# Kernel tuning notes

Hardware: AMD Instinct MI355X
Metric: run time of the kernel (lower is better)

## Reference

```python
import jax, jax.numpy as jnp
import numpy as np
import math

D_MODEL = 1024
NUM_HEADS = 16
D_HEAD = D_MODEL // NUM_HEADS          # 64
N_FREQ = D_HEAD // 2 + 1               # 33 rfft bins
COMPRESSION_RATIO = 0.5


def setup_inputs() -> dict:
    key = jax.random.key(0)
    k_x, k_qkv, k_out, k_b, k_m = jax.random.split(key, 5)
    B, S = 2, 2048
    x = jax.random.normal(k_x, (B, S, D_MODEL), dtype=jnp.float32)
    # Linear weights stored as [in, out] (torch Linear uses [out, in]; math identical).
    w_qkv = jax.random.normal(k_qkv, (D_MODEL, 3 * D_MODEL), dtype=jnp.float32) / math.sqrt(D_MODEL)
    w_out = jax.random.normal(k_out, (D_MODEL, D_MODEL), dtype=jnp.float32) / math.sqrt(D_MODEL)
    b_out = jax.random.normal(k_b, (D_MODEL,), dtype=jnp.float32) * 0.01
    # Learned per-frequency-bin mask logits of AdaptiveFrequencyMask(d_state=d_head).
    # Initialized around logit(compression_ratio) with small noise.
    init_logit = math.log(COMPRESSION_RATIO / (1.0 - COMPRESSION_RATIO))
    mask_logits = init_logit + 0.1 * jax.random.normal(k_m, (N_FREQ,), dtype=jnp.float32)
    return {"x": x, "w_qkv": w_qkv, "w_out": w_out, "b_out": b_out, "mask_logits": mask_logits}


def _spectral_filter(t, mask):
    # rfft over d_head dim, apply learned soft mask, inverse rfft.  t: [B,H,S,dh]
    tf = jnp.fft.rfft(t, axis=-1)          # [B,H,S,N_FREQ] complex
    tf = tf * mask                          # broadcast real mask over bins
    return jnp.fft.irfft(tf, n=t.shape[-1], axis=-1).astype(t.dtype)


def reference(x, w_qkv, w_out, b_out, mask_logits):
    B, S, D = x.shape
    H, dh = NUM_HEADS, D_HEAD
    qkv = x @ w_qkv                                         # [B,S,3D]
    q, k, v = jnp.split(qkv, 3, axis=-1)
    # [B,S,D] -> [B,H,S,dh]
    to_heads = lambda t: t.reshape(B, S, H, dh).transpose(0, 2, 1, 3)
    q, k, v = to_heads(q), to_heads(k), to_heads(v)
    mask = jax.nn.sigmoid(mask_logits)                      # [N_FREQ]
    q = _spectral_filter(q, mask)
    k = _spectral_filter(k, mask)
    scores = jnp.einsum('bhqd,bhkd->bhqk', q, k) / math.sqrt(dh)
    attn = jax.nn.softmax(scores, axis=-1)                  # dropout p=0 (eval)
    out = jnp.einsum('bhqk,bhkd->bhqd', attn, v)
    out = out.transpose(0, 2, 1, 3).reshape(B, S, D)
    return out @ w_out + b_out
```

## Files before the change

kernel.cpp:

```cpp
#include <hip/hip_runtime.h>

#define S_LEN 2048
#define NH    16
#define DH    64
#define DM    1024
#define NQKV  3072

typedef __attribute__((ext_vector_type(8))) __bf16 bf16x8;
typedef __attribute__((ext_vector_type(4))) float  f32x4;
typedef unsigned short ushort_t;

static __device__ __forceinline__ unsigned short bf16b(float f) {
  return __builtin_bit_cast(unsigned short, (__bf16)f);
}

static __device__ __forceinline__ float exp2v(float x) {
  return __builtin_amdgcn_exp2f(x);
}

static __device__ __forceinline__ bf16x8 pack8(float4 f0, float4 f1) {
  uint4 v;
  v.x = ((unsigned)bf16b(f0.y) << 16) | bf16b(f0.x);
  v.y = ((unsigned)bf16b(f0.w) << 16) | bf16b(f0.z);
  v.z = ((unsigned)bf16b(f1.y) << 16) | bf16b(f1.x);
  v.w = ((unsigned)bf16b(f1.w) << 16) | bf16b(f1.z);
  return __builtin_bit_cast(bf16x8, v);
}

static __device__ __forceinline__ void glds16(const void* g, void* l) {
  __builtin_amdgcn_global_load_lds((const __attribute__((address_space(1))) unsigned int*)g,
                                   (__attribute__((address_space(3))) unsigned int*)l, 16, 0, 0);
}

#define OFF_WT  65536ull
#define OFF_WOT 6356992ull
#define OFF_Q   8454144ull
#define OFF_K   16842752ull
#define OFF_V   25231360ull
#define OFF_AO  33619968ull

__global__ __launch_bounds__(256) void k_prep(const float* __restrict__ wqkv,
                                              const float* __restrict__ wout,
                                              const float* __restrict__ x,
                                              const float* __restrict__ logits,
                                              unsigned short* __restrict__ Wt,
                                              unsigned short* __restrict__ Wot,
                                              unsigned short* __restrict__ xb) {
  __shared__ __align__(16) char sbuf[16640];
  int bid = blockIdx.x;
  int t = threadIdx.x;

  if (bid < 256) {
    float* msk = (float*)sbuf;
    float* Kd  = (float*)(sbuf + 144);
    ushort_t (*Fb)[72] = (ushort_t(*)[72])(sbuf + 416);
    if (t < 33) msk[t] = 1.0f / (1.0f + __expf(-logits[t]));
    __syncthreads();
    if (t < 64) {
      float acc = msk[0];
      #pragma unroll
      for (int f = 1; f < 32; ++f) {
        int r = (f * t) & 63;
        acc += 2.0f * msk[f] * __cosf((float)r * (6.28318530717958647692f / 64.0f));
      }
      acc += msk[32] * ((t & 1) ? -1.0f : 1.0f);
      Kd[t] = acc * (1.0f / 64.0f);
    }
    __syncthreads();
    for (int idx = t; idx < 4096; idx += 256) {
      int j = idx >> 6, i = idx & 63;
      Fb[j][i] = bf16b(Kd[(j - i) & 63]);
    }
    __syncthreads();

    int lane = t & 63, w = t >> 6;
    int m16 = lane & 15, quad = lane >> 4;
    int kx = bid >> 5, yy = bid & 31;
    int which = yy >> 4, h = yy & 15;
    int base = which * 1024 + h * 64;

    bf16x8 af0 = *(const bf16x8*)(&Fb[w * 16 + m16][quad * 8]);
    bf16x8 af1 = *(const bf16x8*)(&Fb[w * 16 + m16][32 + quad * 8]);

    f32x4 acc[8] = {};
    #pragma unroll 2
    for (int n = 0; n < 8; ++n) {
      const float* Wg = wqkv + (size_t)(kx * 128 + n * 16 + m16) * NQKV + base + quad * 8;
      float4 a0 = *(const float4*)(Wg);
      float4 a1 = *(const float4*)(Wg + 4);
      float4 b0 = *(const float4*)(Wg + 32);
      float4 b1 = *(const float4*)(Wg + 36);
      acc[n] = __builtin_amdgcn_mfma_f32_16x16x32_bf16(af0, pack8(a0, a1), acc[n], 0, 0, 0);
      acc[n] = __builtin_amdgcn_mfma_f32_16x16x32_bf16(af1, pack8(b0, b1), acc[n], 0, 0, 0);
    }
    float sc = (which == 0) ? 0.18033688011112042f : 1.0f;
    #pragma unroll
    for (int n = 0; n < 8; ++n) {
      #pragma unroll
      for (int r = 0; r < 4; ++r) {
        int j = w * 16 + quad * 4 + r;
        Wt[(size_t)(base + j) * DM + kx * 128 + n * 16 + m16] = bf16b(acc[n][r] * sc);
      }
    }
  } else if (bid < 768) {
    float (*Ts)[65] = (float(*)[65])sbuf;
    int b1 = bid - 256;
    if (b1 < 256) {
      int kt = b1 & 15, nt = b1 >> 4;
      int cb = 2048 + nt * 64, kbase = kt * 64;
      #pragma unroll
      for (int p = 0; p < 16; ++p) {
        int kk = p * 4 + (t >> 6);
        Ts[kk][t & 63] = wqkv[(size_t)(kbase + kk) * NQKV + cb + (t & 63)];
      }
      __syncthreads();
      #pragma unroll
      for (int p = 0; p < 16; ++p) {
        int nn = p * 4 + (t >> 6);
        Wt[(size_t)(cb + nn) * DM + kbase + (t & 63)] = bf16b(Ts[t & 63][nn]);
      }
    } else {
      int b2 = b1 - 256;
      int kt = b2 & 15, nt = b2 >> 4;
      int cb = nt * 64, kbase = kt * 64;
      #pragma unroll
      for (int p = 0; p < 16; ++p) {
        int kk = p * 4 + (t >> 6);
        Ts[kk][t & 63] = wout[(size_t)(kbase + kk) * DM + cb + (t & 63)];
      }
      __syncthreads();
      #pragma unroll
      for (int p = 0; p < 16; ++p) {
        int nn = p * 4 + (t >> 6);
        Wot[(size_t)(cb + nn) * DM + kbase + (t & 63)] = bf16b(Ts[t & 63][nn]);
      }
    }
  } else {
    size_t i = ((size_t)(bid - 768) * 256 + t) * 8;
    const float4* xp = (const float4*)(x + i);
    float4 a = xp[0], b = xp[1];
    uint4 v;
    v.x = ((unsigned)bf16b(a.y) << 16) | bf16b(a.x);
    v.y = ((unsigned)bf16b(a.w) << 16) | bf16b(a.z);
    v.z = ((unsigned)bf16b(b.y) << 16) | bf16b(b.x);
    v.w = ((unsigned)bf16b(b.w) << 16) | bf16b(b.z);
    *(uint4*)(xb + i) = v;
  }
}

template<int BM, int BN, int WCOLS, int MR, int NR>
__device__ __forceinline__ void gemm_core2(const unsigned short* __restrict__ A,
                                           const unsigned short* __restrict__ Bw,
                                           int bm, int bn, unsigned short* smem,
                                           f32x4 (&acc)[MR][NR]) {
  constexpr int SLOT = (BM + BN) * 64;
  constexpr int PA = BM / 64, PB = BN / 64;
  constexpr int L = PA + PB;
  int t = threadIdx.x, lane = t & 63, w = t >> 6;
  int m16 = lane & 15, quad = lane >> 4;
  int wr = (w / WCOLS) * (MR * 16), wc = (w % WCOLS) * (NR * 16);
  int xr = m16 & 7;
  int trow = t >> 3, tcol = t & 7;
  int gsw = (tcol ^ (trow & 7)) * 8;
  const unsigned short* Ag = A  + (size_t)(bm * BM + trow) * DM + gsw;
  const unsigned short* Bg = Bw + (size_t)(bn * BN + trow) * DM + gsw;
  unsigned short* Al = smem + trow * 64 + tcol * 8;
  unsigned short* Bl = smem + BM * 64 + trow * 64 + tcol * 8;

  #pragma unroll
  for (int s = 0; s < 2; ++s) {
    #pragma unroll
    for (int p = 0; p < PA; ++p)
      glds16(Ag + (size_t)p * 64 * DM + s * 64, Al + s * SLOT + p * 4096);
    #pragma unroll
    for (int p = 0; p < PB; ++p)
      glds16(Bg + (size_t)p * 64 * DM + s * 64, Bl + s * SLOT + p * 4096);
  }

  #pragma unroll 1
  for (int ks = 0; ks < 16; ++ks) {
    if (ks < 15) asm volatile("s_waitcnt vmcnt(%0)" :: "n"(L) : "memory");
    else         asm volatile("s_waitcnt vmcnt(0)" ::: "memory");
    __builtin_amdgcn_s_barrier();
    __builtin_amdgcn_sched_barrier(0);
    const unsigned short* As = smem + (ks & 1) * SLOT;
    const unsigned short* Bs = As + BM * 64;
    #pragma unroll
    for (int kk = 0; kk < 2; ++kk) {
      bf16x8 af[MR], bfr[NR];
      #pragma unroll
      for (int i = 0; i < MR; ++i)
        af[i] = *(const bf16x8*)(As + (wr + i * 16 + m16) * 64 + ((kk * 4 + quad) ^ xr) * 8);
      #pragma unroll
      for (int j = 0; j < NR; ++j)
        bfr[j] = *(const bf16x8*)(Bs + (wc + j * 16 + m16) * 64 + ((kk * 4 + quad) ^ xr) * 8);
      #pragma unroll
      for (int i = 0; i < MR; ++i)
        #pragma unroll
        for (int j = 0; j < NR; ++j)
          acc[i][j] = __builtin_amdgcn_mfma_f32_16x16x32_bf16(af[i], bfr[j], acc[i][j], 0, 0, 0);
    }
    if (ks < 14) {
      __builtin_amdgcn_s_barrier();
      __builtin_amdgcn_sched_barrier(0);
      int kn = ks + 2;
      #pragma unroll
      for (int p = 0; p < PA; ++p)
        glds16(Ag + (size_t)p * 64 * DM + kn * 64, Al + (ks & 1) * SLOT + p * 4096);
      #pragma unroll
      for (int p = 0; p < PB; ++p)
        glds16(Bg + (size_t)p * 64 * DM + kn * 64, Bl + (ks & 1) * SLOT + p * 4096);
    }
  }
  __syncthreads();
}

__global__ __launch_bounds__(512, 1) void k_gemm_qkv(const unsigned short* __restrict__ xb,
                                                     const unsigned short* __restrict__ Bw,
                                                     unsigned short* __restrict__ Qb,
                                                     unsigned short* __restrict__ Kb,
                                                     unsigned short* __restrict__ Vt) {
  __shared__ __align__(16) unsigned short smem[65536];
  f32x4 acc[8][4] = {};
  int bn = blockIdx.x, bm = blockIdx.y;
  gemm_core2<256, 256, 4, 8, 4>(xb, Bw, bm, bn, smem, acc);

  int t = threadIdx.x, lane = t & 63, w = t >> 6;
  int m16 = lane & 15, quad = lane >> 4;
  int b = bm >> 3, srow = (bm & 7) * 256;
  int which = bn >> 2;
  ushort_t (*Tr)[264] = (ushort_t(*)[264])smem;

  if (which < 2) {
    unsigned short* dstB = which ? Kb : Qb;
    int hbase = (bn & 3) * 4;
    #pragma unroll
    for (int ch = 0; ch < 2; ++ch) {
      if ((w >> 2) == ch) {
        #pragma unroll
        for (int i = 0; i < 8; ++i)
          #pragma unroll
          for (int j = 0; j < 4; ++j)
            #pragma unroll
            for (int r = 0; r < 4; ++r)
              Tr[i * 16 + quad * 4 + r][(w & 3) * 64 + j * 16 + m16] = bf16b(acc[i][j][r]);
      }
      __syncthreads();
      int row = t >> 2, qh = t & 3;
      unsigned short* dst = dstB +
          ((size_t)(b * 16 + hbase + qh) * 2048 + srow + ch * 128 + row) * 64;
      #pragma unroll
      for (int p = 0; p < 8; ++p)
        *(uint4*)(dst + p * 8) = *(const uint4*)(&Tr[row][qh * 64 + p * 8]);
      __syncthreads();
    }
  } else {
    int hb = (bn - 8) * 4;
    #pragma unroll
    for (int ch = 0; ch < 2; ++ch) {
      if (((w >> 1) & 1) == ch) {
        #pragma unroll
        for (int i = 0; i < 8; ++i)
          #pragma unroll
          for (int j = 0; j < 4; ++j)
            #pragma unroll
            for (int r = 0; r < 4; ++r)
              Tr[(w & 1) * 64 + j * 16 + m16][(w >> 2) * 128 + i * 16 + quad * 4 + r] =
                  bf16b(acc[i][j][r]);
      }
      __syncthreads();
      int c = t >> 2, qh = t & 3;
      int h = hb + ch * 2 + (c >> 6), d = c & 63;
      unsigned short* dst = Vt + ((size_t)(b * 16 + h) * 64 + d) * 2048 + srow;
      #pragma unroll
      for (int p = 0; p < 8; ++p)
        *(uint4*)(dst + qh * 64 + p * 8) = *(const uint4*)(&Tr[c][qh * 64 + p * 8]);
      __syncthreads();
    }
  }
}

__global__ __launch_bounds__(512, 2) void k_attn(const unsigned short* __restrict__ Qb,
                                                 const unsigned short* __restrict__ Kb,
                                                 const unsigned short* __restrict__ Vt,
                                                 unsigned short* __restrict__ AO) {
  __shared__ __align__(16) unsigned short smem[65536];
  int t = threadIdx.x;
  int w = t >> 6, lane = t & 63;
  int m16 = lane & 15, quad = lane >> 4;
  int bid = blockIdx.x;
  int jj = bid >> 3;
  int bh = ((jj & 3) << 3) + (bid & 7);
  int qbase = (jj >> 2) * 256 + w * 32;

  const unsigned short* QpA = Qb + ((size_t)bh * S_LEN + qbase + m16) * DH + quad * 8;
  const unsigned short* QpB = QpA + 16 * DH;
  bf16x8 aq0A = *(const bf16x8*)(QpA);
  bf16x8 aq1A = *(const bf16x8*)(QpA + 32);
  bf16x8 aq0B = *(const bf16x8*)(QpB);
  bf16x8 aq1B = *(const bf16x8*)(QpB + 32);
  const unsigned short* Kbase = Kb + (size_t)bh * S_LEN * DH;
  const unsigned short* Vbase = Vt + (size_t)bh * DH * S_LEN;

  int xr = m16 & 7;
  unsigned short* Pw = smem + 32768 + w * 4096;

  int trow = t >> 3;
  int tcol = t & 7;
  int gswz = tcol ^ (trow & 7);
  const unsigned short* Kg = Kbase + (size_t)trow * 64 + gswz * 8;
  const unsigned short* Vg = Vbase + (size_t)trow * S_LEN + gswz * 8;
  unsigned short* Kl = smem + trow * 64 + tcol * 8;
  unsigned short* Vl = smem + 16384 + trow * 64 + tcol * 8;

  f32x4 oA[4] = {}, oB[4] = {};
  float lA = 0.f, lB = 0.f;
  f32x4 zero = {0.f, 0.f, 0.f, 0.f};

  #pragma unroll
  for (int tt = 0; tt < 4; ++tt) {
    glds16(Kg + (size_t)tt * 4096, Kl + tt * 4096);
    glds16(Vg + tt * 64,           Vl + tt * 4096);
  }

  #pragma unroll 1
  for (int wnd = 0; wnd < 16; ++wnd) {
    if (wnd < 15) asm volatile("s_waitcnt vmcnt(4)" ::: "memory");
    else          asm volatile("s_waitcnt vmcnt(0)" ::: "memory");
    __builtin_amdgcn_s_barrier();
    __builtin_amdgcn_sched_barrier(0);
    int sb = (wnd & 1) << 1;
    const unsigned short* Ka  = smem + sb * 4096;
    const unsigned short* Kbs = smem + (sb + 1) * 4096;
    const unsigned short* Va  = smem + 16384 + sb * 4096;
    const unsigned short* Vbs = smem + 16384 + (sb + 1) * 4096;
    unsigned short* Pa = Pw;
    unsigned short* Pb = Pw + 2048;

    f32x4 saA[4], saB[4];
    #pragma unroll
    for (int g = 0; g < 4; ++g) {
      int rk = g * 16 + m16;
      bf16x8 kf0 = *(const bf16x8*)(Ka + rk * 64 + ((quad ^ xr) * 8));
      bf16x8 kf1 = *(const bf16x8*)(Ka + rk * 64 + (((4 + quad) ^ xr) * 8));
      saA[g] = __builtin_amdgcn_mfma_f32_16x16x32_bf16(kf0, aq0A, zero, 0, 0, 0);
      saA[g] = __builtin_amdgcn_mfma_f32_16x16x32_bf16(kf1, aq1A, saA[g], 0, 0, 0);
      saB[g] = __builtin_amdgcn_mfma_f32_16x16x32_bf16(kf0, aq0B, zero, 0, 0, 0);
      saB[g] = __builtin_amdgcn_mfma_f32_16x16x32_bf16(kf1, aq1B, saB[g], 0, 0, 0);
    }
    #pragma unroll
    for (int g = 0; g < 4; ++g) {
      int chw = (((2 * g + (quad >> 1)) ^ xr) << 3) + ((quad & 1) << 2);
      float a0 = exp2v(saA[g][0]), a1 = exp2v(saA[g][1]);
      float a2 = exp2v(saA[g][2]), a3 = exp2v(saA[g][3]);
      lA += (a0 + a1) + (a2 + a3);
      uint2 pka;
      pka.x = ((unsigned)bf16b(a1) << 16) | bf16b(a0);
      pka.y = ((unsigned)bf16b(a3) << 16) | bf16b(a2);
      *(uint2*)(Pa + m16 * 64 + chw) = pka;
      float b0 = exp2v(saB[g][0]), b1 = exp2v(saB[g][1]);
      float b2 = exp2v(saB[g][2]), b3 = exp2v(saB[g][3]);
      lB += (b0 + b1) + (b2 + b3);
      uint2 pkb;
      pkb.x = ((unsigned)bf16b(b1) << 16) | bf16b(b0);
      pkb.y = ((unsigned)bf16b(b3) << 16) | bf16b(b2);
      *(uint2*)(Pa + (16 + m16) * 64 + chw) = pkb;
    }
    f32x4 sbA[4], sbB[4];
    #pragma unroll
    for (int g = 0; g < 4; ++g) {
      int rk = g * 16 + m16;
      bf16x8 kf0 = *(const bf16x8*)(Kbs + rk * 64 + ((quad ^ xr) * 8));
      bf16x8 kf1 = *(const bf16x8*)(Kbs + rk * 64 + (((4 + quad) ^ xr) * 8));
      sbA[g] = __builtin_amdgcn_mfma_f32_16x16x32_bf16(kf0, aq0A, zero, 0, 0, 0);
      sbA[g] = __builtin_amdgcn_mfma_f32_16x16x32_bf16(kf1, aq1A, sbA[g], 0, 0, 0);
      sbB[g] = __builtin_amdgcn_mfma_f32_16x16x32_bf16(kf0, aq0B, zero, 0, 0, 0);
      sbB[g] = __builtin_amdgcn_mfma_f32_16x16x32_bf16(kf1, aq1B, sbB[g], 0, 0, 0);
    }
    #pragma unroll
    for (int c = 0; c < 2; ++c) {
      bf16x8 apA = *(const bf16x8*)(Pa + m16 * 64 + (((4 * c + quad) ^ xr) << 3));
      bf16x8 apB = *(const bf16x8*)(Pa + (16 + m16) * 64 + (((4 * c + quad) ^ xr) << 3));
      #pragma unroll
      for (int j = 0; j < 4; ++j) {
        int dv = j * 16 + m16;
        bf16x8 bv = *(const bf16x8*)(Va + dv * 64 + (((c * 4 + quad) ^ xr) * 8));
        oA[j] = __builtin_amdgcn_mfma_f32_16x16x32_bf16(apA, bv, oA[j], 0, 0, 0);
        oB[j] = __builtin_amdgcn_mfma_f32_16x16x32_bf16(apB, bv, oB[j], 0, 0, 0);
      }
    }
    #pragma unroll
    for (int g = 0; g < 4; ++g) {
      int chw = (((2 * g + (quad >> 1)) ^ xr) << 3) + ((quad & 1) << 2);
      float a0 = exp2v(sbA[g][0]), a1 = exp2v(sbA[g][1]);
      float a2 = exp2v(sbA[g][2]), a3 = exp2v(sbA[g][3]);
      lA += (a0 + a1) + (a2 + a3);
      uint2 pka;
      pka.x = ((unsigned)bf16b(a1) << 16) | bf16b(a0);
      pka.y = ((unsigned)bf16b(a3) << 16) | bf16b(a2);
      *(uint2*)(Pb + m16 * 64 + chw) = pka;
      float b0 = exp2v(sbB[g][0]), b1 = exp2v(sbB[g][1]);
      float b2 = exp2v(sbB[g][2]), b3 = exp2v(sbB[g][3]);
      lB += (b0 + b1) + (b2 + b3);
      uint2 pkb;
      pkb.x = ((unsigned)bf16b(b1) << 16) | bf16b(b0);
      pkb.y = ((unsigned)bf16b(b3) << 16) | bf16b(b2);
      *(uint2*)(Pb + (16 + m16) * 64 + chw) = pkb;
    }
    #pragma unroll
    for (int c = 0; c < 2; ++c) {
      bf16x8 apA = *(const bf16x8*)(Pb + m16 * 64 + (((4 * c + quad) ^ xr) << 3));
      bf16x8 apB = *(const bf16x8*)(Pb + (16 + m16) * 64 + (((4 * c + quad) ^ xr) << 3));
      #pragma unroll
      for (int j = 0; j < 4; ++j) {
        int dv = j * 16 + m16;
        bf16x8 bv = *(const bf16x8*)(Vbs + dv * 64 + (((c * 4 + quad) ^ xr) * 8));
        oA[j] = __builtin_amdgcn_mfma_f32_16x16x32_bf16(apA, bv, oA[j], 0, 0, 0);
        oB[j] = __builtin_amdgcn_mfma_f32_16x16x32_bf16(apB, bv, oB[j], 0, 0, 0);
      }
    }
    if (wnd < 14) {
      __builtin_amdgcn_s_barrier();
      int ta = 2 * wnd + 4;
      glds16(Kg + (size_t)ta * 4096,       Kl + sb * 4096);
      glds16(Vg + ta * 64,                 Vl + sb * 4096);
      glds16(Kg + (size_t)(ta + 1) * 4096, Kl + (sb + 1) * 4096);
      glds16(Vg + (ta + 1) * 64,           Vl + (sb + 1) * 4096);
    }
  }

  lA += __shfl_xor(lA, 16); lA += __shfl_xor(lA, 32);
  lB += __shfl_xor(lB, 16); lB += __shfl_xor(lB, 32);
  float ivA = 1.0f / lA;
  float ivB = 1.0f / lB;
  int b = bh >> 4, h = bh & 15;
  #pragma unroll
  for (int r = 0; r < 4; ++r) {
    float vA = __shfl(ivA, quad * 4 + r);
    float vB = __shfl(ivB, quad * 4 + r);
    size_t row0 = (size_t)b * S_LEN + qbase + quad * 4 + r;
    unsigned short* d0 = AO + row0 * DM + h * DH + m16;
    unsigned short* d1 = AO + (row0 + 16) * DM + h * DH + m16;
    #pragma unroll
    for (int j = 0; j < 4; ++j) {
      d0[j * 16] = bf16b(oA[j][r] * vA);
      d1[j * 16] = bf16b(oB[j][r] * vB);
    }
  }
}

__global__ __launch_bounds__(512, 1) void k_gemm_out(const unsigned short* __restrict__ A,
                                                     const unsigned short* __restrict__ Bw,
                                                     const float* __restrict__ bias,
                                                     float* __restrict__ out) {
  __shared__ __align__(16) unsigned short smem[49152];
  f32x4 acc[4][4] = {};
  int bn = blockIdx.x, bm = blockIdx.y;
  gemm_core2<256, 128, 2, 4, 4>(A, Bw, bm, bn, smem, acc);

  int t = threadIdx.x, lane = t & 63, w = t >> 6;
  int m16 = lane & 15, quad = lane >> 4;
  int wr = (w >> 1) * 64, wc = (w & 1) * 64;
  #pragma unroll
  for (int i = 0; i < 4; ++i) {
    int grow = bm * 256 + wr + i * 16 + quad * 4;
    #pragma unroll
    for (int j = 0; j < 4; ++j) {
      int gc = bn * 128 + wc + j * 16 + m16;
      float bb = bias[gc];
      #pragma unroll
      for (int r = 0; r < 4; ++r)
        out[(size_t)(grow + r) * DM + gc] = acc[i][j][r] + bb;
    }
  }
}

extern "C" void kernel_launch(void* const* d_in, const int* in_sizes, int n_in,
                              void* d_out, int out_size, void* d_ws, size_t ws_size,
                              hipStream_t stream) {
  const float* x    = (const float*)d_in[0];
  const float* wqkv = (const float*)d_in[1];
  const float* wout = (const float*)d_in[2];
  const float* bout = (const float*)d_in[3];
  const float* mlog = (const float*)d_in[4];
  char* ws = (char*)d_ws;
  unsigned short* Wt  = (unsigned short*)(ws + OFF_WT);
  unsigned short* Wot = (unsigned short*)(ws + OFF_WOT);
  unsigned short* Qb  = (unsigned short*)(ws + OFF_Q);
  unsigned short* Kb  = (unsigned short*)(ws + OFF_K);
  unsigned short* Vt  = (unsigned short*)(ws + OFF_V);
  unsigned short* xb  = (unsigned short*)(ws + OFF_AO);
  unsigned short* AO  = (unsigned short*)(ws + OFF_AO);
  float* out = (float*)d_out;

  k_prep<<<dim3(2816), dim3(256), 0, stream>>>(wqkv, wout, x, mlog, Wt, Wot, xb);
  k_gemm_qkv<<<dim3(12, 16), dim3(512), 0, stream>>>(xb, Wt, Qb, Kb, Vt);
  k_attn<<<dim3(256), dim3(512), 0, stream>>>(Qb, Kb, Vt, AO);
  k_gemm_out<<<dim3(8, 16), dim3(512), 0, stream>>>(AO, Wot, bout, out);
}
```

Before: 189.9 us.

## Keep attention probabilities in registers via key permutation; shrink out-proj tiles

The attention kernel loads K rows in a permuted order (with a matching global swizzle), so each lane's QK^T MFMA outputs line up with the A-operand layout of the PV MFMA. The probabilities can then be packed straight into registers, dropping the per-wave LDS scratch for P, its writes and reads, and halving the attention kernel's shared memory. Separately, the output projection GEMM moves from 256x128 to 128x128 tiles with twice as many blocks, to fill more CUs. The register-resident P raises register pressure, and the smaller GEMM tiles lower data reuse.

```diff
diff --git a/kernel.cpp b/kernel.cpp
--- a/kernel.cpp
+++ b/kernel.cpp
@@ -284,7 +284,7 @@
                                                  const unsigned short* __restrict__ Kb,
                                                  const unsigned short* __restrict__ Vt,
                                                  unsigned short* __restrict__ AO) {
-  __shared__ __align__(16) unsigned short smem[65536];
+  __shared__ __align__(16) unsigned short smem[32768];
   int t = threadIdx.x;
   int w = t >> 6, lane = t & 63;
   int m16 = lane & 15, quad = lane >> 4;
@@ -303,13 +303,14 @@
   const unsigned short* Vbase = Vt + (size_t)bh * DH * S_LEN;
 
   int xr = m16 & 7;
-  unsigned short* Pw = smem + 32768 + w * 4096;
+  int krow0 = ((m16 >> 2) << 3) + (m16 & 3);
 
   int trow = t >> 3;
   int tcol = t & 7;
-  int gswz = tcol ^ (trow & 7);
-  const unsigned short* Kg = Kbase + (size_t)trow * 64 + gswz * 8;
-  const unsigned short* Vg = Vbase + (size_t)trow * S_LEN + gswz * 8;
+  int gswzK = tcol ^ ((trow & 3) | ((trow >> 1) & 4));
+  int gswzV = tcol ^ (trow & 7);
+  const unsigned short* Kg = Kbase + (size_t)trow * 64 + gswzK * 8;
+  const unsigned short* Vg = Vbase + (size_t)trow * S_LEN + gswzV * 8;
   unsigned short* Kl = smem + trow * 64 + tcol * 8;
   unsigned short* Vl = smem + 16384 + trow * 64 + tcol * 8;
 
@@ -322,6 +323,60 @@
     glds16(Kg + (size_t)tt * 4096, Kl + tt * 4096);
     glds16(Vg + tt * 64,           Vl + tt * 4096);
   }
+
+#define QK_TILE(KSH, SA, SB)                                                              \
+    _Pragma("unroll")                                                                     \
+    for (int c = 0; c < 2; ++c) {                                                         \
+      _Pragma("unroll")                                                                   \
+      for (int gl = 0; gl < 2; ++gl) {                                                    \
+        int key = c * 32 + krow0 + gl * 4;                                                \
+        bf16x8 kf0 = *(const bf16x8*)((KSH) + key * 64 + ((quad ^ xr) * 8));              \
+        bf16x8 kf1 = *(const bf16x8*)((KSH) + key * 64 + (((4 + quad) ^ xr) * 8));        \
+        SA[c][gl] = __builtin_amdgcn_mfma_f32_16x16x32_bf16(kf0, aq0A, zero, 0, 0, 0);    \
+        SA[c][gl] = __builtin_amdgcn_mfma_f32_16x16x32_bf16(kf1, aq1A, SA[c][gl], 0, 0, 0);\
+        SB[c][gl] = __builtin_amdgcn_mfma_f32_16x16x32_bf16(kf0, aq0B, zero, 0, 0, 0);    \
+        SB[c][gl] = __builtin_amdgcn_mfma_f32_16x16x32_bf16(kf1, aq1B, SB[c][gl], 0, 0, 0);\
+      }                                                                                   \
+    }
+
+#define SM_TILE(SA, SB, PA_, PB_)                                                         \
+    _Pragma("unroll")                                                                     \
+    for (int c = 0; c < 2; ++c) {                                                         \
+      float a0 = exp2v(SA[c][0][0]), a1 = exp2v(SA[c][0][1]);                             \
+      float a2 = exp2v(SA[c][0][2]), a3 = exp2v(SA[c][0][3]);                             \
+      float a4 = exp2v(SA[c][1][0]), a5 = exp2v(SA[c][1][1]);                             \
+      float a6 = exp2v(SA[c][1][2]), a7 = exp2v(SA[c][1][3]);                             \
+      lA += ((a0 + a1) + (a2 + a3)) + ((a4 + a5) + (a6 + a7));                            \
+      uint4 ua;                                                                           \
+      ua.x = ((unsigned)bf16b(a1) << 16) | bf16b(a0);                                     \
+      ua.y = ((unsigned)bf16b(a3) << 16) | bf16b(a2);                                     \
+      ua.z = ((unsigned)bf16b(a5) << 16) | bf16b(a4);                                     \
+      ua.w = ((unsigned)bf16b(a7) << 16) | bf16b(a6);                                     \
+      PA_[c] = __builtin_bit_cast(bf16x8, ua);                                            \
+      float b0 = exp2v(SB[c][0][0]), b1 = exp2v(SB[c][0][1]);                             \
+      float b2 = exp2v(SB[c][0][2]), b3 = exp2v(SB[c][0][3]);                             \
+      float b4 = exp2v(SB[c][1][0]), b5 = exp2v(SB[c][1][1]);                             \
+      float b6 = exp2v(SB[c][1][2]), b7 = exp2v(SB[c][1][3]);                             \
+      lB += ((b0 + b1) + (b2 + b3)) + ((b4 + b5) + (b6 + b7));                            \
+      uint4 ub;                                                                           \
+      ub.x = ((unsigned)bf16b(b1) << 16) | bf16b(b0);                                     \
+      ub.y = ((unsigned)bf16b(b3) << 16) | bf16b(b2);                                     \
+      ub.z = ((unsigned)bf16b(b5) << 16) | bf16b(b4);                                     \
+      ub.w = ((unsigned)bf16b(b7) << 16) | bf16b(b6);                                     \
+      PB_[c] = __builtin_bit_cast(bf16x8, ub);                                            \
+    }
+
+#define PV_TILE(VSH, PA_, PB_)                                                            \
+    _Pragma("unroll")                                                                     \
+    for (int c = 0; c < 2; ++c) {                                                         \
+      _Pragma("unroll")                                                                   \
+      for (int j = 0; j < 4; ++j) {                                                       \
+        int dv = j * 16 + m16;                                                            \
+        bf16x8 bv = *(const bf16x8*)((VSH) + dv * 64 + (((c * 4 + quad) ^ xr) * 8));      \
+        oA[j] = __builtin_amdgcn_mfma_f32_16x16x32_bf16(PA_[c], bv, oA[j], 0, 0, 0);      \
+        oB[j] = __builtin_amdgcn_mfma_f32_16x16x32_bf16(PB_[c], bv, oB[j], 0, 0, 0);      \
+      }                                                                                   \
+    }
 
   #pragma unroll 1
   for (int wnd = 0; wnd < 16; ++wnd) {
@@ -334,91 +389,18 @@
     const unsigned short* Kbs = smem + (sb + 1) * 4096;
     const unsigned short* Va  = smem + 16384 + sb * 4096;
     const unsigned short* Vbs = smem + 16384 + (sb + 1) * 4096;
-    unsigned short* Pa = Pw;
-    unsigned short* Pb = Pw + 2048;
-
-    f32x4 saA[4], saB[4];
-    #pragma unroll
-    for (int g = 0; g < 4; ++g) {
-      int rk = g * 16 + m16;
-      bf16x8 kf0 = *(const bf16x8*)(Ka + rk * 64 + ((quad ^ xr) * 8));
-      bf16x8 kf1 = *(const bf16x8*)(Ka + rk * 64 + (((4 + quad) ^ xr) * 8));
-      saA[g] = __builtin_amdgcn_mfma_f32_16x16x32_bf16(kf0, aq0A, zero, 0, 0, 0);
-      saA[g] = __builtin_amdgcn_mfma_f32_16x16x32_bf16(kf1, aq1A, saA[g], 0, 0, 0);
-      saB[g] = __builtin_amdgcn_mfma_f32_16x16x32_bf16(kf0, aq0B, zero, 0, 0, 0);
-      saB[g] = __builtin_amdgcn_mfma_f32_16x16x32_bf16(kf1, aq1B, saB[g], 0, 0, 0);
-    }
-    #pragma unroll
-    for (int g = 0; g < 4; ++g) {
-      int chw = (((2 * g + (quad >> 1)) ^ xr) << 3) + ((quad & 1) << 2);
-      float a0 = exp2v(saA[g][0]), a1 = exp2v(saA[g][1]);
-      float a2 = exp2v(saA[g][2]), a3 = exp2v(saA[g][3]);
-      lA += (a0 + a1) + (a2 + a3);
-      uint2 pka;
-      pka.x = ((unsigned)bf16b(a1) << 16) | bf16b(a0);
-      pka.y = ((unsigned)bf16b(a3) << 16) | bf16b(a2);
-      *(uint2*)(Pa + m16 * 64 + chw) = pka;
-      float b0 = exp2v(saB[g][0]), b1 = exp2v(saB[g][1]);
-      float b2 = exp2v(saB[g][2]), b3 = exp2v(saB[g][3]);
-      lB += (b0 + b1) + (b2 + b3);
-      uint2 pkb;
-      pkb.x = ((unsigned)bf16b(b1) << 16) | bf16b(b0);
-      pkb.y = ((unsigned)bf16b(b3) << 16) | bf16b(b2);
-      *(uint2*)(Pa + (16 + m16) * 64 + chw) = pkb;
-    }
-    f32x4 sbA[4], sbB[4];
-    #pragma unroll
-    for (int g = 0; g < 4; ++g) {
-      int rk = g * 16 + m16;
-      bf16x8 kf0 = *(const bf16x8*)(Kbs + rk * 64 + ((quad ^ xr) * 8));
-      bf16x8 kf1 = *(const bf16x8*)(Kbs + rk * 64 + (((4 + quad) ^ xr) * 8));
-      sbA[g] = __builtin_amdgcn_mfma_f32_16x16x32_bf16(kf0, aq0A, zero, 0, 0, 0);
-      sbA[g] = __builtin_amdgcn_mfma_f32_16x16x32_bf16(kf1, aq1A, sbA[g], 0, 0, 0);
-      sbB[g] = __builtin_amdgcn_mfma_f32_16x16x32_bf16(kf0, aq0B, zero, 0, 0, 0);
-      sbB[g] = __builtin_amdgcn_mfma_f32_16x16x32_bf16(kf1, aq1B, sbB[g], 0, 0, 0);
-    }
-    #pragma unroll
-    for (int c = 0; c < 2; ++c) {
-      bf16x8 apA = *(const bf16x8*)(Pa + m16 * 64 + (((4 * c + quad) ^ xr) << 3));
-      bf16x8 apB = *(const bf16x8*)(Pa + (16 + m16) * 64 + (((4 * c + quad) ^ xr) << 3));
-      #pragma unroll
-      for (int j = 0; j < 4; ++j) {
-        int dv = j * 16 + m16;
-        bf16x8 bv = *(const bf16x8*)(Va + dv * 64 + (((c * 4 + quad) ^ xr) * 8));
-        oA[j] = __builtin_amdgcn_mfma_f32_16x16x32_bf16(apA, bv, oA[j], 0, 0, 0);
-        oB[j] = __builtin_amdgcn_mfma_f32_16x16x32_bf16(apB, bv, oB[j], 0, 0, 0);
-      }
-    }
-    #pragma unroll
-    for (int g = 0; g < 4; ++g) {
-      int chw = (((2 * g + (quad >> 1)) ^ xr) << 3) + ((quad & 1) << 2);
-      float a0 = exp2v(sbA[g][0]), a1 = exp2v(sbA[g][1]);
-      float a2 = exp2v(sbA[g][2]), a3 = exp2v(sbA[g][3]);
-      lA += (a0 + a1) + (a2 + a3);
-      uint2 pka;
-      pka.x = ((unsigned)bf16b(a1) << 16) | bf16b(a0);
-      pka.y = ((unsigned)bf16b(a3) << 16) | bf16b(a2);
-      *(uint2*)(Pb + m16 * 64 + chw) = pka;
-      float b0 = exp2v(sbB[g][0]), b1 = exp2v(sbB[g][1]);
-      float b2 = exp2v(sbB[g][2]), b3 = exp2v(sbB[g][3]);
-      lB += (b0 + b1) + (b2 + b3);
-      uint2 pkb;
-      pkb.x = ((unsigned)bf16b(b1) << 16) | bf16b(b0);
-      pkb.y = ((unsigned)bf16b(b3) << 16) | bf16b(b2);
-      *(uint2*)(Pb + (16 + m16) * 64 + chw) = pkb;
-    }
-    #pragma unroll
-    for (int c = 0; c < 2; ++c) {
-      bf16x8 apA = *(const bf16x8*)(Pb + m16 * 64 + (((4 * c + quad) ^ xr) << 3));
-      bf16x8 apB = *(const bf16x8*)(Pb + (16 + m16) * 64 + (((4 * c + quad) ^ xr) << 3));
-      #pragma unroll
-      for (int j = 0; j < 4; ++j) {
-        int dv = j * 16 + m16;
-        bf16x8 bv = *(const bf16x8*)(Vbs + dv * 64 + (((c * 4 + quad) ^ xr) * 8));
-        oA[j] = __builtin_amdgcn_mfma_f32_16x16x32_bf16(apA, bv, oA[j], 0, 0, 0);
-        oB[j] = __builtin_amdgcn_mfma_f32_16x16x32_bf16(apB, bv, oB[j], 0, 0, 0);
-      }
-    }
+
+    f32x4 sA[2][2], sB[2][2];
+    QK_TILE(Ka, sA, sB)
+    bf16x8 paA[2], paB[2];
+    SM_TILE(sA, sB, paA, paB)
+    f32x4 tA[2][2], tB[2][2];
+    QK_TILE(Kbs, tA, tB)
+    PV_TILE(Va, paA, paB)
+    bf16x8 pbA[2], pbB[2];
+    SM_TILE(tA, tB, pbA, pbB)
+    PV_TILE(Vbs, pbA, pbB)
+
     if (wnd < 14) {
       __builtin_amdgcn_s_barrier();
       int ta = 2 * wnd + 4;
@@ -428,6 +410,9 @@
       glds16(Vg + (ta + 1) * 64,           Vl + (sb + 1) * 4096);
     }
   }
+#undef QK_TILE
+#undef SM_TILE
+#undef PV_TILE
 
   lA += __shfl_xor(lA, 16); lA += __shfl_xor(lA, 32);
   lB += __shfl_xor(lB, 16); lB += __shfl_xor(lB, 32);
@@ -453,19 +438,19 @@
                                                      const unsigned short* __restrict__ Bw,
                                                      const float* __restrict__ bias,
                                                      float* __restrict__ out) {
-  __shared__ __align__(16) unsigned short smem[49152];
-  f32x4 acc[4][4] = {};
+  __shared__ __align__(16) unsigned short smem[32768];
+  f32x4 acc[4][2] = {};
   int bn = blockIdx.x, bm = blockIdx.y;
-  gemm_core2<256, 128, 2, 4, 4>(A, Bw, bm, bn, smem, acc);
+  gemm_core2<128, 128, 4, 4, 2>(A, Bw, bm, bn, smem, acc);
 
   int t = threadIdx.x, lane = t & 63, w = t >> 6;
   int m16 = lane & 15, quad = lane >> 4;
-  int wr = (w >> 1) * 64, wc = (w & 1) * 64;
+  int wr = (w >> 2) * 64, wc = (w & 3) * 32;
   #pragma unroll
   for (int i = 0; i < 4; ++i) {
-    int grow = bm * 256 + wr + i * 16 + quad * 4;
-    #pragma unroll
-    for (int j = 0; j < 4; ++j) {
+    int grow = bm * 128 + wr + i * 16 + quad * 4;
+    #pragma unroll
+    for (int j = 0; j < 2; ++j) {
       int gc = bn * 128 + wc + j * 16 + m16;
       float bb = bias[gc];
       #pragma unroll
@@ -496,5 +481,5 @@
   k_prep<<<dim3(2816), dim3(256), 0, stream>>>(wqkv, wout, x, mlog, Wt, Wot, xb);
   k_gemm_qkv<<<dim3(12, 16), dim3(512), 0, stream>>>(xb, Wt, Qb, Kb, Vt);
   k_attn<<<dim3(256), dim3(512), 0, stream>>>(Qb, Kb, Vt, AO);
-  k_gemm_out<<<dim3(8, 16), dim3(512), 0, stream>>>(AO, Wot, bout, out);
-}
+  k_gemm_out<<<dim3(8, 32), dim3(512), 0, stream>>>(AO, Wot, bout, out);
+}
```

Result: faster. 185.0 us (-2.6%).
